# Kernel optimization log

Measured on AMD Instinct MI355X. Metric: run time of the kernel, lower is better.

The kernel has to match this reference:

```python
import jax, jax.numpy as jnp
import numpy as np

K_NEIGHBORS = 3
CLASSES = 5


def _l2_norm(x):
    # x: (N, C, H, W) -> (N, H*W, C), unit L2 norm over channel dim
    N, C, H, W = x.shape
    x = x.reshape(N, C, H * W).transpose(0, 2, 1)
    return x / jnp.linalg.norm(x, axis=-1, keepdims=True)


def setup_inputs() -> dict:
    key = jax.random.key(0)
    k1, k2 = jax.random.split(key)
    anchor = jax.random.normal(k1, (32, 64, 21, 21), dtype=jnp.float32)
    support_set = jax.random.normal(k2, (25, 64, 21, 21), dtype=jnp.float32)
    return {"anchor": anchor, "support_set": support_set, "av_num": 1, "sav_num": 1}


def reference(anchor, support_set, av_num, sav_num):
    # anchor: (B*AV, C, H, W), support_set: (L*S, C, H, W)
    q = _l2_norm(anchor)            # (B, HW, C)
    s = _l2_norm(support_set)       # (L*S, HW, C)
    C = s.shape[-1]
    s_flat = s.reshape(-1, C)       # (M, C), M = L*S*HW (class-major)
    # dense cosine similarity: (B, HW, M)
    sim = jnp.einsum('bqc,mc->bqm', q, s_flat)
    B, HW, M = sim.shape
    per_cls = M // CLASSES
    # (B//av, av, HW, L, S*HW)
    sim = sim.reshape(B // av_num, av_num, HW, CLASSES, per_cls)
    sim = jax.nn.sigmoid(sim)
    # av_num == 1 -> squeeze AV dim (matches torch squeeze(1) path)
    sim = sim[:, 0] if av_num == 1 else jnp.power(jnp.prod(sim, axis=1), 1.0 / av_num)
    # per-class top-k over descriptors, sum over k and over query locations
    topk = jax.lax.top_k(sim, K_NEIGHBORS)[0]        # (B, HW, L, K)
    i2c_sim = topk.sum(axis=-1).sum(axis=-2)         # (B, L)
    return i2c_sim
```

## Files before the change

kernel.cpp:

```cpp
#include <hip/hip_runtime.h>
#include <hip/hip_bf16.h>
#include <math.h>

#define CLASSES     5
#define C_DIM       64
#define HW          441
#define B_ANCH      32
#define NSUP        25
#define NROWS       (B_ANCH*HW)
#define MSUP        (NSUP*HW)
#define PER_CLS     (MSUP/CLASSES)
#define TILE_COLS   64
#define PER_CLS_PAD 2304
#define NPAD        (PER_CLS_PAD - PER_CLS)
#define ROW_BYTES   (C_DIM*2)
#define QUARTERS    4
#define ROWS_PER_BLK 128
#define NBLK_X      ((NROWS + ROWS_PER_BLK - 1) / ROWS_PER_BLK)

#define NEG_INF  (-1e30f)

typedef __bf16 bf16x8 __attribute__((ext_vector_type(8)));
typedef float  f32x4  __attribute__((ext_vector_type(4)));

#define TOP3_INS(v, t0, t1, t2) do {                              \
    float _v = (v);                                               \
    float _n0 = fmaxf(_v, (t0));                                  \
    float _n1 = __builtin_amdgcn_fmed3f(_v, (t0), (t1));          \
    float _n2 = __builtin_amdgcn_fmed3f(_v, (t1), (t2));          \
    (t0) = _n0; (t1) = _n1; (t2) = _n2; } while (0)

typedef __attribute__((address_space(1))) const void g_void;
typedef __attribute__((address_space(3))) void l_void;
__device__ __forceinline__ void gload_lds16(const void* g, void* l) {
    __builtin_amdgcn_global_lo\
ad_lds((g_void*)g, (l_void*)l, 16, 0, 0);
}

__global__ __launch_bounds__(256) void norm_rows_kernel(
    const float* __restrict__ anchor, const float* __restrict__ support,
    __bf16* __restrict__ qb, __bf16* __restrict__ sb) {
    int r = blockIdx.x * 256 + threadIdx.x;
    const int total_main = MSUP + NROWS;
    if (r >= total_main) {
        int i = r - total_main;
        if (i < CLASSES * NPAD) {
            int cls = i / NPAD, ix = PER_CLS + i % NPAD;
            __bf16* op = sb + ((size_t)cls * PER_CLS_PAD + ix) * C_DIM;
            bf16x8 z = {};
            #pragma unroll
            for (int c0 = 0; c0 < C_DIM; c0 += 8) *(bf16x8*)(op + c0) = z;
        }
        return;
    }
    bool isSup = r < MSUP;
    int rc = isSup ? r : r - MSUP;
    const float* in = isSup ? support : anchor;
    int img = rc / HW, p = rc % HW;
    const float* base = in + (size_t)img * C_DIM * HW + p;
    float q[C_DIM];
    float ss = 0.f;
    #pragma unroll
    for (int c = 0; c < C_DIM; ++c) { q[c] = base[c * HW]; ss += q[c] * q[c]; }
    float sc = rsqrtf(ss);
    __bf16* op;
    if (isSup) {
        int cls = rc / PER_CLS, ix = rc - cls * PER_CLS;
        op = sb + ((size_t)cls * PER_CLS_PAD + ix) * C_DIM;
    } else {
        op = qb + (size_t)rc * C_DIM;
    }
    #pragma unroll
    for (int c0 = 0; c0 < C_DIM; c0 += 8) {
        bf16x8 v;
        #pragma unroll
        for (int j = 0; j < 8; ++j) v[j] = (__bf16)(q[c0 + j] * sc);
        *(bf16x8*)(op + c0) = v;
    }
}

template<int QNT, bool TAIL>
__device__ __forceinline__ void gemm_quarter(
    const char* qbase,
    char* smem_base,
    int laneOff,
    int pr0, int lane, int lr,
    const bf16x8 a0[2], const bf16x8 a1[2],
    float t0[2][4], float t1[2][4], float t2[2][4]) {

    auto stage = [&](int buf, int tt) {
        const char* tb = qbase + tt * (TILE_COLS * ROW_BYTES);
        #pragma unroll
        for (int i = 0; i < 2; ++i) {
            int pr = pr0 + 4 * i;
            gload_lds16(tb + ((pr >> 1) * 2048 + (pr & 1) * 64) + laneOff,
                        smem_base + buf * 8192 + pr * 1024);
        }
    };

    const bf16x8* sm = (const bf16x8*)smem_base;
    const f32x4 z = {0.f, 0.f, 0.f, 0.f};

    stage(0, 0);
    stage(1, 1);
    #pragma unroll
    for (int tt = 0; tt < QNT; ++tt) {
        if (tt < QNT - 1) asm volatile("s_waitcnt vmcnt(2)" ::: "memory");
        else              asm volatile("s_waitcnt vmcnt(0)" ::: "memory");
        __builtin_amdgcn_s_barrier();
        if (tt + 2 < QNT) stage((tt + 2) % 3, tt + 2);
        const int buf = tt % 3;
        const bool tail = TAIL && (tt == QNT - 1);
        __builtin_amdgcn_s_setprio(1);
        if (!tail) {
            bf16x8 b[8];
            #pragma unroll
            for (int s = 0; s < 4; ++s) {
                b[2*s]   = sm[((buf*4 + s)*2 + 0)*64 + lane];
                b[2*s+1] = sm[((buf*4 + s)*2 + 1)*64 + lane];
            }
            #pragma unroll
            for (int s = 0; s < 4; ++s)
                #pragma unroll
                for (int r = 0; r < 2; ++r) {
                    f32x4 acc = __builtin_amdgcn_mfma_f32_16x16x32_bf16(
                        a0[r], b[2*s], z, 0, 0, 0);
                    acc = __builtin_amdgcn_mfma_f32_16x16x32_bf16(
                        a1[r], b[2*s+1], acc, 0, 0, 0);
                    #pragma unroll
                    for (int j = 0; j < 4; ++j)
                        TOP3_INS(acc[j], t0[r][j], t1[r][j], t2[r][j]);
                }
        } else {
            #pragma unroll
            for (int s = 0; s < 2; ++s) {
                bf16x8 b0 = sm[((buf*4 + s)*2 + 0)*64 + lane];
                bf16x8 b1 = sm[((buf*4 + s)*2 + 1)*64 + lane];
                bool valid = (s == 0) || (lr < 13);
                #pragma unroll
                for (int r = 0; r < 2; ++r) {
                    f32x4 acc = __builtin_amdgcn_mfma_f32_16x16x32_bf16(
                        a0[r], b0, z, 0, 0, 0);
                    acc = __builtin_amdgcn_mfma_f32_16x16x32_bf16(
                        a1[r], b1, acc, 0, 0, 0);
                    #pragma unroll
                    for (int j = 0; j < 4; ++j) {
                        float v = valid ? acc[j] : NEG_INF;
                        TOP3_INS(v, t0[r][j], t1[r][j], t2[r][j]);
                    }
                }
            }
        }
        __builtin_amdgcn_s_setprio(0);
    }
}

__global__ __launch_bounds__(256) void knn_mfma_kernel(
    const __bf16* __restrict__ qb, const __bf16* __restrict__ sb,
    float* __restrict__ part) {
    __shared__ bf16x8 smem[3][4][2][64];

    int lane = threadIdx.x & 63;
    int w    = threadIdx.x >> 6;
    int lr   = lane & 15;
    int kg   = lane >> 4;
    int cls  = blockIdx.y >> 2;
    int q    = blockIdx.y & 3;
    int rowbase = blockIdx.x * ROWS_PER_BLK + w * 32;

    bf16x8 a0[2], a1[2];
    #pragma unroll
    for (int r = 0; r < 2; ++r) {
        int arow = rowbase + r * 16 + lr;
        int arc  = arow < NROWS ? arow : NROWS - 1;
        const bf16x8* qrow = (const bf16x8*)(qb + (size_t)arc * C_DIM);
        a0[r] = qrow[kg];
        a1[r] = qrow[4 + kg];
    }

    float t0[2][4], t1[2][4], t2[2][4];
    #pragma unroll
    for (int r = 0; r < 2; ++r)
        #pragma unroll
        for (int j = 0; j < 4; ++j) {
            t0[r][j] = NEG_INF; t1[r][j] = NEG_INF; t2[r][j] = NEG_INF;
        }

    const char* qbase = (const char*)sb
        + (size_t)cls * PER_CLS_PAD * ROW_BYTES
        + (size_t)q * 9 * (TILE_COLS * ROW_BYTES);
    int laneOff = lr * ROW_BYTES + kg * 16;

    if (q == 3)
        gemm_quarter<8, true >(qbase, (char*)smem, laneOff, w, lane, lr,
                               a0, a1, t0, t1, t2);
    else
        gemm_quarter<9, false>(qbase, (char*)smem, laneOff, w, lane, lr,
                               a0, a1, t0, t1, t2);

    #pragma unroll
    for (int r = 0; r < 2; ++r) {
        #pragma unroll
        for (int j = 0; j < 4; ++j) {
            float u0 = t0[r][j], u1 = t1[r][j], u2 = t2[r][j];
            #pragma unroll
            for (int off = 1; off < 16; off <<= 1) {
                float v0 = __shfl_xor(u0, off, 64);
                float v1 = __shfl_xor(u1, off, 64);
                float v2 = __shfl_xor(u2, off, 64);
                TOP3_INS(v0, u0, u1, u2);
                TOP3_INS(v1, u0, u1, u2);
                TOP3_INS(v2, u0, u1, u2);
            }
            int row = rowbase + r * 16 + kg * 4 + j;
            if (lr == 0 && row < NROWS) {
                float* pp = part +
                    ((size_t)(row * CLASSES + cls) * QUARTERS + q) * 3;
                pp[0] = u0; pp[1] = u1; pp[2] = u2;
            }
        }
    }
}

__global__ __launch_bounds__(64) void merge_reduce_kernel(
    const float* __restrict__ part, float* __restrict__ out) {
    int bl = blockIdx.x;
    int b = bl / CLASSES;
    int l = bl % CLASSES;
    int lane = threadIdx.x;
    float acc = 0.f;
    for (int p = lane; p < HW; p += 64) {
        int row = b * HW + p;
        const float* pp = part + (size_t)(row * CLASSES + l) * (QUARTERS * 3);
        float u0 = NEG_INF, u1 = NEG_INF, u2 = NEG_INF;
        #pragma unroll
        for (int k = 0; k < QUARTERS * 3; ++k) TOP3_INS(pp[k], u0, u1, u2);
        acc += 1.f / (1.f + __expf(-u0))
             + 1.f / (1.f + __expf(-u1))
             + 1.f / (1.f + __expf(-u2));
    }
    #pragma unroll
    for (int off = 32; off; off >>= 1) acc += __shfl_xor(acc, off, 64);
    if (lane == 0) out[bl] = acc;
}

extern "C" void kernel_launch(void* const* d_in, const int* in_sizes, int n_in,
                              void* d_out, int out_size, void* d_ws, size_t ws_size,
                              hipStream_t stream) {
    const float* anchor  = (const float*)d_in[0];
    const float* support = (const float*)d_in[1];

    __bf16* sb = (__bf16*)d_ws;
    __bf16* qb = sb + (size_t)CLASSES * PER_CLS_PAD * C_DIM;
    float* part = (float*)(qb + (size_t)NROWS * C_DIM);

    {
        int total = MSUP + NROWS + CLASSES * NPAD;
        dim3 g((total + 255) / 256);
        norm_rows_kernel<<<g, 256, 0, stream>>>(anchor, support, qb, sb);
    }
    {
        dim3 g(NBLK_X, CLASSES * QUARTERS);
        knn_mfma_kernel<<<g, 256, 0, stream>>>(qb, sb, part);
    }
    {
        dim3 gm(B_ANCH * CLASSES);
        merge_reduce_kernel<<<gm, 64, 0, stream>>>(part, (float*)d_out);
    }
}
```

Measured before the change: 57.25 us.

## Replace LDS staging with direct per-wave register loads and merge top-3 lists

Removes the shared-memory triple-buffered staging of support tiles, which used global_load_lds and a barrier per tile. Each wave now loads its B fragments straight from global memory into registers, with a three-slot software pipeline over 32-column halves. Top-3 merging in the shuffle reduction and in the final merge kernel now uses a closed-form sorted-triple merge instead of three sequential inserts. This drops barriers and LDS traffic, but all four waves in a block now fetch the same support data separately through cache, and the register buffers raise register pressure.

```diff
diff --git a/kernel.cpp b/kernel.cpp
--- a/kernel.cpp
+++ b/kernel.cpp
@@ -10,10 +10,10 @@
 #define NROWS       (B_ANCH*HW)
 #define MSUP        (NSUP*HW)
 #define PER_CLS     (MSUP/CLASSES)
-#define TILE_COLS   64
 #define PER_CLS_PAD 2304
 #define NPAD        (PER_CLS_PAD - PER_CLS)
 #define ROW_BYTES   (C_DIM*2)
+#define HALF_BYTES  (32*ROW_BYTES)
 #define QUARTERS    4
 #define ROWS_PER_BLK 128
 #define NBLK_X      ((NROWS + ROWS_PER_BLK - 1) / ROWS_PER_BLK)
@@ -30,12 +30,14 @@
     float _n2 = __builtin_amdgcn_fmed3f(_v, (t1), (t2));          \
     (t0) = _n0; (t1) = _n1; (t2) = _n2; } while (0)
 
-typedef __attribute__((address_space(1))) const void g_void;
-typedef __attribute__((address_space(3))) void l_void;
-__device__ __forceinline__ void gload_lds16(const void* g, void* l) {
-    __builtin_amdgcn_global_lo\
-ad_lds((g_void*)g, (l_void*)l, 16, 0, 0);
-}
+#define TRIPLE_MERGE(u0, u1, u2, v0, v1, v2) do {                 \
+    float _A = fminf((u0), (v0));                                 \
+    float _B = fmaxf((u1), (v1));                                 \
+    float _E = fmaxf((u2), (v2));                                 \
+    float _m0 = fmaxf((u0), (v0));                                \
+    float _m1 = __builtin_amdgcn_fmed3f((u0), (v0), _B);          \
+    float _m2 = __builtin_amdgcn_fmed3f(_A, _B, _E);              \
+    (u0) = _m0; (u1) = _m1; (u2) = _m2; } while (0)
 
 __global__ __launch_bounds__(256) void norm_rows_kernel(
     const float* __restrict__ anchor, const float* __restrict__ support,
@@ -79,87 +81,61 @@
     }
 }
 
-template<int QNT, bool TAIL>
-__device__ __forceinline__ void gemm_quarter(
-    const char* qbase,
-    char* smem_base,
-    int laneOff,
-    int pr0, int lane, int lr,
+template<int NH, bool TAIL>
+__device__ __forceinline__ void scan_quarter(
+    const char* __restrict__ hb, int lr,
     const bf16x8 a0[2], const bf16x8 a1[2],
     float t0[2][4], float t1[2][4], float t2[2][4]) {
-
-    auto stage = [&](int buf, int tt) {
-        const char* tb = qbase + tt * (TILE_COLS * ROW_BYTES);
-        #pragma unroll
-        for (int i = 0; i < 2; ++i) {
-            int pr = pr0 + 4 * i;
-            gload_lds16(tb + ((pr >> 1) * 2048 + (pr & 1) * 64) + laneOff,
-                        smem_base + buf * 8192 + pr * 1024);
-        }
+    const f32x4 z = {0.f, 0.f, 0.f, 0.f};
+    bf16x8 B0[4], B1[4], B2[4];
+
+    auto load_half = [&](bf16x8 (&d)[4], int h) {
+        #pragma unroll
+        for (int f = 0; f < 4; ++f)
+            d[f] = *(const bf16x8*)(hb + (size_t)h * HALF_BYTES
+                                      + (f >> 1) * 2048 + (f & 1) * 64);
     };
-
-    const bf16x8* sm = (const bf16x8*)smem_base;
-    const f32x4 z = {0.f, 0.f, 0.f, 0.f};
-
-    stage(0, 0);
-    stage(1, 1);
-    #pragma unroll
-    for (int tt = 0; tt < QNT; ++tt) {
-        if (tt < QNT - 1) asm volatile("s_waitcnt vmcnt(2)" ::: "memory");
-        else              asm volatile("s_waitcnt vmcnt(0)" ::: "memory");
-        __builtin_amdgcn_s_barrier();
-        if (tt + 2 < QNT) stage((tt + 2) % 3, tt + 2);
-        const int buf = tt % 3;
-        const bool tail = TAIL && (tt == QNT - 1);
-        __builtin_amdgcn_s_setprio(1);
-        if (!tail) {
-            bf16x8 b[8];
+    auto comp_half = [&](const bf16x8 (&s)[4], int h) {
+        #pragma unroll
+        for (int cf = 0; cf < 2; ++cf) {
+            bool masked = TAIL && (h == NH - 1) && (cf == 1);
             #pragma unroll
-            for (int s = 0; s < 4; ++s) {
-                b[2*s]   = sm[((buf*4 + s)*2 + 0)*64 + lane];
-                b[2*s+1] = sm[((buf*4 + s)*2 + 1)*64 + lane];
-            }
-            #pragma unroll
-            for (int s = 0; s < 4; ++s)
-                #pragma unroll
-                for (int r = 0; r < 2; ++r) {
-                    f32x4 acc = __builtin_amdgcn_mfma_f32_16x16x32_bf16(
-                        a0[r], b[2*s], z, 0, 0, 0);
-                    acc = __builtin_amdgcn_mfma_f32_16x16x32_bf16(
-                        a1[r], b[2*s+1], acc, 0, 0, 0);
-                    #pragma unroll
-                    for (int j = 0; j < 4; ++j)
-                        TOP3_INS(acc[j], t0[r][j], t1[r][j], t2[r][j]);
-                }
-        } else {
-            #pragma unroll
-            for (int s = 0; s < 2; ++s) {
-                bf16x8 b0 = sm[((buf*4 + s)*2 + 0)*64 + lane];
-                bf16x8 b1 = sm[((buf*4 + s)*2 + 1)*64 + lane];
-                bool valid = (s == 0) || (lr < 13);
-                #pragma unroll
-                for (int r = 0; r < 2; ++r) {
-                    f32x4 acc = __builtin_amdgcn_mfma_f32_16x16x32_bf16(
-                        a0[r], b0, z, 0, 0, 0);
-                    acc = __builtin_amdgcn_mfma_f32_16x16x32_bf16(
-                        a1[r], b1, acc, 0, 0, 0);
+            for (int r = 0; r < 2; ++r) {
+                f32x4 acc = __builtin_amdgcn_mfma_f32_16x16x32_bf16(
+                    a0[r], s[cf * 2 + 0], z, 0, 0, 0);
+                acc = __builtin_amdgcn_mfma_f32_16x16x32_bf16(
+                    a1[r], s[cf * 2 + 1], acc, 0, 0, 0);
+                if (masked) {
+                    bool valid = lr < 13;
                     #pragma unroll
                     for (int j = 0; j < 4; ++j) {
                         float v = valid ? acc[j] : NEG_INF;
                         TOP3_INS(v, t0[r][j], t1[r][j], t2[r][j]);
                     }
+                } else {
+                    #pragma unroll
+                    for (int j = 0; j < 4; ++j)
+                        TOP3_INS(acc[j], t0[r][j], t1[r][j], t2[r][j]);
                 }
             }
         }
-        __builtin_amdgcn_s_setprio(0);
+    };
+
+    load_half(B0, 0);
+    load_half(B1, 1);
+    #pragma unroll
+    for (int h = 0; h < NH; ++h) {
+        switch (h % 3) {
+            case 0: if (h + 2 < NH) load_half(B2, h + 2); comp_half(B0, h); break;
+            case 1: if (h + 2 < NH) load_half(B0, h + 2); comp_half(B1, h); break;
+            default:if (h + 2 < NH) load_half(B1, h + 2); comp_half(B2, h); break;
+        }
     }
 }
 
 __global__ __launch_bounds__(256) void knn_mfma_kernel(
     const __bf16* __restrict__ qb, const __bf16* __restrict__ sb,
     float* __restrict__ part) {
-    __shared__ bf16x8 smem[3][4][2][64];
-
     int lane = threadIdx.x & 63;
     int w    = threadIdx.x >> 6;
     int lr   = lane & 15;
@@ -186,17 +162,15 @@
             t0[r][j] = NEG_INF; t1[r][j] = NEG_INF; t2[r][j] = NEG_INF;
         }
 
-    const char* qbase = (const char*)sb
+    const char* hb = (const char*)sb
         + (size_t)cls * PER_CLS_PAD * ROW_BYTES
-        + (size_t)q * 9 * (TILE_COLS * ROW_BYTES);
-    int laneOff = lr * ROW_BYTES + kg * 16;
+        + (size_t)q * 18 * HALF_BYTES
+        + lr * ROW_BYTES + kg * 16;
 
     if (q == 3)
-        gemm_quarter<8, true >(qbase, (char*)smem, laneOff, w, lane, lr,
-                               a0, a1, t0, t1, t2);
+        scan_quarter<15, true >(hb, lr, a0, a1, t0, t1, t2);
     else
-        gemm_quarter<9, false>(qbase, (char*)smem, laneOff, w, lane, lr,
-                               a0, a1, t0, t1, t2);
+        scan_quarter<18, false>(hb, lr, a0, a1, t0, t1, t2);
 
     #pragma unroll
     for (int r = 0; r < 2; ++r) {
@@ -208,9 +182,7 @@
                 float v0 = __shfl_xor(u0, off, 64);
                 float v1 = __shfl_xor(u1, off, 64);
                 float v2 = __shfl_xor(u2, off, 64);
-                TOP3_INS(v0, u0, u1, u2);
-                TOP3_INS(v1, u0, u1, u2);
-                TOP3_INS(v2, u0, u1, u2);
+                TRIPLE_MERGE(u0, u1, u2, v0, v1, v2);
             }
             int row = rowbase + r * 16 + kg * 4 + j;
             if (lr == 0 && row < NROWS) {
@@ -232,9 +204,10 @@
     for (int p = lane; p < HW; p += 64) {
         int row = b * HW + p;
         const float* pp = part + (size_t)(row * CLASSES + l) * (QUARTERS * 3);
-        float u0 = NEG_INF, u1 = NEG_INF, u2 = NEG_INF;
-        #pragma unroll
-        for (int k = 0; k < QUARTERS * 3; ++k) TOP3_INS(pp[k], u0, u1, u2);
+        float u0 = pp[0], u1 = pp[1], u2 = pp[2];
+        TRIPLE_MERGE(u0, u1, u2, pp[3], pp[4],  pp[5]);
+        TRIPLE_MERGE(u0, u1, u2, pp[6], pp[7],  pp[8]);
+        TRIPLE_MERGE(u0, u1, u2, pp[9], pp[10], pp[11]);
         acc += 1.f / (1.f + __expf(-u0))
              + 1.f / (1.f + __expf(-u1))
              + 1.f / (1.f + __expf(-u2));
```

Result: slower. 95.37 us (+66.6%).
